# Optimization experiments

Hardware: AMD Instinct MI355X
Metric: run time of the kernel (lower is better)

The kernel has to match this reference:

```python
import jax, jax.numpy as jnp
import numpy as np

D_EMB = 1024
N_HEADS = 16
HEAD_SIZE = 64
LN_EPS = 1e-5


def _layernorm(x, g, b):
    mu = jnp.mean(x, axis=-1, keepdims=True)
    var = jnp.var(x, axis=-1, keepdims=True)
    return (x - mu) * jax.lax.rsqrt(var + LN_EPS) * g + b


def setup_inputs() -> dict:
    key = jax.random.key(0)
    ks = jax.random.split(key, 16)
    B, N, D, H, HS = 8, 1024, D_EMB, N_HEADS, HEAD_SIZE
    s_in = 1.0 / np.sqrt(D)
    s_h = 1.0 / np.sqrt(H * HS)
    s_ff = 1.0 / np.sqrt(4 * D)
    return {
        "x": jax.random.normal(ks[0], (B, N, D), jnp.float32),
        # per-head q/k/v projections, stacked over heads: [H, D, HS]
        "Wq": jax.random.normal(ks[1], (H, D, HS), jnp.float32) * s_in,
        "bq": jnp.zeros((H, HS), jnp.float32),
        "Wk": jax.random.normal(ks[2], (H, D, HS), jnp.float32) * s_in,
        "bk": jnp.zeros((H, HS), jnp.float32),
        "Wv": jax.random.normal(ks[3], (H, D, HS), jnp.float32) * s_in,
        "bv": jnp.zeros((H, HS), jnp.float32),
        "Wproj": jax.random.normal(ks[4], (H * HS, D), jnp.float32) * s_h,
        "bproj": jnp.zeros((D,), jnp.float32),
        "W1": jax.random.normal(ks[5], (D, 4 * D), jnp.float32) * s_in,
        "b1": jnp.zeros((4 * D,), jnp.float32),
        "W2": jax.random.normal(ks[6], (4 * D, D), jnp.float32) * s_ff,
        "b2": jnp.zeros((D,), jnp.float32),
        "ln1_g": jnp.ones((D,), jnp.float32),
        "ln1_b": jnp.zeros((D,), jnp.float32),
        "ln2_g": jnp.ones((D,), jnp.float32),
        "ln2_b": jnp.zeros((D,), jnp.float32),
    }


def reference(x, Wq, bq, Wk, bk, Wv, bv, Wproj, bproj, W1, b1, W2, b2,
              ln1_g, ln1_b, ln2_g, ln2_b):
    # --- pre-LN multi-head attention (dropout = identity in eval) ---
    h = _layernorm(x, ln1_g, ln1_b)                    # [B, N, D]
    q = jnp.einsum('bnd,hds->bhns', h, Wq) + bq[None, :, None, :]
    k = jnp.einsum('bnd,hds->bhns', h, Wk) + bk[None, :, None, :]
    v = jnp.einsum('bnd,hds->bhns', h, Wv) + bv[None, :, None, :]
    scale = 1.0 / jnp.sqrt(jnp.float32(HEAD_SIZE))
    wei = jnp.einsum('bhns,bhms->bhnm', q, k) * scale  # [B, H, N, N]
    wei = jax.nn.softmax(wei, axis=-1)
    attn = jnp.einsum('bhnm,bhms->bhns', wei, v)       # [B, H, N, HS]
    B, H, N, HS = attn.shape
    attn = attn.transpose(0, 2, 1, 3).reshape(B, N, H * HS)  # concat heads
    x = x + attn @ Wproj + bproj
    # --- pre-LN feed-forward with LeakyReLU ---
    h2 = _layernorm(x, ln2_g, ln2_b)
    ff = jax.nn.leaky_relu(h2 @ W1 + b1, negative_slope=0.01) @ W2 + b2
    return x + ff
```

## Files before the change

kernel.cpp:

```cpp
#include <hip/hip_runtime.h>
#include <cstdint>
#include <cstddef>

typedef unsigned short u16;
typedef __attribute__((ext_vector_type(4))) float f32x4;
typedef __attribute__((ext_vector_type(8))) short s16x8;

#define D_EMB 1024
#define NSEQ 1024
#define NB 8
#define NH 16
#define HS 64
#define DFF 4096
#define MTOT (NB*NSEQ)

__device__ __forceinline__ u16 f2bf(float f){
  unsigned u = __float_as_uint(f);
  u += 0x7FFFu + ((u >> 16) & 1u);
  return (u16)(u >> 16);
}
__device__ __forceinline__ u16 bft(float f){ return (u16)(__float_as_uint(f) >> 16); }

__device__ __forceinline__ void gload_lds16(const void* g, void* l){
  __builtin_amdgcn_global_load_lds((const __attribute__((address_space(1))) void*)g,
                                   (__attribute__((address_space(3))) void*)l, 16, 0, 0);
}

__global__ void transpose_cvt(const float* __restrict__ in, u16* __restrict__ out,
                              int R, int C, size_t inStride, size_t outStride){
  __shared__ float t[32][33];
  const float* ip = in + (size_t)blockIdx.z * inStride;
  u16* op = out + (size_t)blockIdx.z * outStride;
  int c0 = blockIdx.x * 32, r0 = blockIdx.y * 32;
  int tx = threadIdx.x, ty = threadIdx.y;
#pragma unroll
  for (int j = 0; j < 32; j += 8)
    t[ty + j][tx] = ip[(size_t)(r0 + ty + j) * C + (c0 + tx)];
  __syncthreads();
#pragma unroll
  for (int j = 0; j < 32; j += 8)
    op[(size_t)(c0 + ty + j) * R + (r0 + tx)] = f2bf(t[tx][ty + j]);
}

__global__ __launch_bounds__(256) void ln_kernel(const float* __restrict__ x,
    const float* __restrict__ g, const float* __restrict__ bb, u16* __restrict__ out){
  int row = blockIdx.x;
  const float* xr = x + (size_t)row * D_EMB;
  int c = threadIdx.x * 4;
  f32x4 v = *(const f32x4*)(xr + c);
  float s1 = v[0] + v[1] + v[2] + v[3];
  float s2 = v[0]*v[0] + v[1]*v[1] + v[2]*v[2] + v[3]*v[3];
#pragma unroll
  for (int m = 32; m > 0; m >>= 1){ s1 += __shfl_xor(s1, m); s2 += __shfl_xor(s2, m); }
  __shared__ float ps1[4], ps2[4];
  int w = threadIdx.x >> 6;
  if ((threadIdx.x & 63) == 0){ ps1[w] = s1; ps2[w] = s2; }
  __syncthreads();
  s1 = ps1[0] + ps1[1] + ps1[2] + ps1[3];
  s2 = ps2[0] + ps2[1] + ps2[2] + ps2[3];
  float mu = s1 * (1.f / D_EMB);
  float var = s2 * (1.f / D_EMB) - mu * mu;
  float rs = rsqrtf(var + 1e-5f);
  ushort4 o;
  o.x = f2bf((v[0]-mu)*rs*g[c+0] + bb[c+0]);
  o.y = f2bf((v[1]-mu)*rs*g[c+1] + bb[c+1]);
  o.z = f2bf((v[2]-mu)*rs*g[c+2] + bb[c+2]);
  o.w = f2bf((v[3]-mu)*rs*g[c+3] + bb[c+3]);
  *(ushort4*)(out + (size_t)row * D_EMB + c) = o;
}

template<int MODE, int BMT, int BNT, int NTHR>
__global__ __launch_bounds__(NTHR) void gemm2ph(
    const u16* __restrict__ A, const u16* __restrict__ Bt,
    int M, int N, int K,
    const float* __restrict__ bias0, const float* __restrict__ bias1,
    const float* __restrict__ bias2, const float* __restrict__ resid,
    void* __restrict__ o0, void* __restrict__ o1, void* __restrict__ o2)
{
  constexpr int NWAVE = NTHR/64;
  constexpr int WCN = BNT/64, WRN = NWAVE/WCN;
  constexpr int WROWS = BMT/WRN;
  constexpr int RF = WROWS/16;
  static_assert(RF*16*WRN == BMT, "wave tiling must cover BMT");
  constexpr int RPP = NTHR/4;
  constexpr int ALD = (BMT*32)/(NTHR*8);
  constexpr int BLD = (BNT*32)/(NTHR*8);
  __shared__ alignas(16) u16 Al[2][BMT*32];
  __shared__ alignas(16) u16 Bl[2][BNT*32];

  const int tid = threadIdx.x;
  const int wid = tid>>6, lane = tid&63, lr = lane&15, lg = lane>>4;
  const int wr = wid/WCN, wc = wid%WCN;

  const int gx = gridDim.x;
  const int gy = gridDim.y;
  const int nwg = gx * gy;
  const int bid = blockIdx.x + blockIdx.y*gx;
  const int wg = (bid&7)*(nwg>>3) + (bid>>3);
  const int m0 = (wg / gy) * BMT;
  const int n0 = (wg % gy) * BNT;

  const int srow = tid>>2;
  const int scs = (((tid&3) - ((srow>>1)&3)) & 3) * 8;

  auto stage = [&](int buf, int kt){
    const u16* asrc = A + (size_t)(m0 + srow)*K + kt*32 + scs;
#pragma unroll
    for (int r = 0; r < ALD; ++r)
      gload_lds16(asrc + (size_t)(r*RPP)*K, &Al[buf][r*(NTHR*8) + tid*8]);
    const u16* bsrc = Bt + (size_t)(n0 + srow)*K + kt*32 + scs;
#pragma unroll
    for (int r = 0; r < BLD; ++r)
      gload_lds16(bsrc + (size_t)(r*RPP)*K, &Bl[buf][r*(NTHR*8) + tid*8]);
  };

  f32x4 acc[RF][4];
#pragma unroll
  for (int i = 0; i < RF; i++)
#pragma unroll
    for (int j = 0; j < 4; j++) acc[i][j] = {0.f,0.f,0.f,0.f};

  const int nk = K/32;
  stage(0, 0);
  for (int kt = 0; kt < nk; ++kt){
    __syncthreads();
    if (kt + 1 < nk) stage((kt+1)&1, kt+1);
    const int buf = kt & 1;
    s16x8 af[RF], bf[4];
#pragma unroll
    for (int i = 0; i < RF; i++){
      const int ar = wr*WROWS + i*16 + lr;
      af[i] = *(const s16x8*)&Al[buf][ar*32 + (((lg + (ar>>1)) & 3)<<3)];
    }
#pragma unroll
    for (int j = 0; j < 4; j++){
      const int br = wc*64 + j*16 + lr;
      bf[j] = *(const s16x8*)&Bl[buf][br*32 + (((lg + (br>>1)) & 3)<<3)];
    }
#pragma unroll
    for (int i = 0; i < RF; i++)
#pragma unroll
      for (int j = 0; j < 4; j++)
        acc[i][j] = __builtin_amdgcn_mfma_f32_16x16x32_bf16(af[i], bf[j], acc[i][j], 0, 0, 0);
  }

#pragma unroll
  for (int fm = 0; fm < RF; fm++){
    const int gmb = m0 + wr*WROWS + fm*16 + lg*4;
#pragma unroll
    for (int fn = 0; fn < 4; fn++){
      const int gn = n0 + wc*64 + fn*16 + lr;
#pragma unroll
      for (int i = 0; i < 4; i++){
        const int gm = gmb + i;
        float v = acc[fm][fn][i];
        if (MODE == 0){
          const int cls = gn >> 10, nn = gn & 1023;
          if (cls == 0)      ((u16*)o0)[(size_t)gm * D_EMB + nn] = f2bf((v + bias0[nn]) * 0.18033688f);
          else if (cls == 1) ((u16*)o1)[(size_t)gm * D_EMB + nn] = f2bf(v + bias1[nn]);
          else {
            const int hh = nn >> 6, ss = nn & 63, bb = gm >> 10, tt = gm & 1023;
            ((u16*)o2)[(((size_t)(bb * NH + hh)) * HS + ss) * NSEQ + tt] = f2bf(v + bias2[nn]);
          }
        } else if (MODE == 1){
          ((float*)o0)[(size_t)gm * N + gn] = resid[(size_t)gm * N + gn] + v + bias0[gn];
        } else {
          float y = v + bias0[gn];
          y = y > 0.f ? y : 0.01f * y;
          ((u16*)o0)[(size_t)gm * N + gn] = f2bf(y);
        }
      }
    }
  }
}

__global__ __launch_bounds__(256) void attn_kernel(
    const u16* __restrict__ Qb, const u16* __restrict__ Kb, const u16* __restrict__ VT,
    u16* __restrict__ attnC)
{
  const int bid = blockIdx.x;
  const int bh = bid & 127, qt = bid >> 7;
  const int b = bh >> 4, h = bh & 15;
  const int tid = threadIdx.x, w = tid >> 6, lane = tid & 63;
  const int lr = lane & 15, lg = lane >> 4;
  const int q0 = qt * 128 + w * 32;

  __shared__ alignas(16) u16 Kl[2][64*64];
  __shared__ alignas(16) u16 Vl[2][64*64];
  __shared__ alignas(16) u16 Pl[4][32][72];

  const int srow = tid >> 3, scg = tid & 7;
  const u16* kbase = Kb + (size_t)(b * NSEQ) * D_EMB + h * HS;
  const u16* vbase = VT + ((size_t)(b * NH + h)) * HS * NSEQ;

  auto stage = [&](int buf, int kt){
    const int tk = kt * 64;
#pragma unroll
    for (int p = 0; p < 2; ++p){
      const int row = srow + p * 32;
      const int sc = scg ^ (row & 7);
      gload_lds16(kbase + (size_t)(tk + row) * D_EMB + sc * 8, &Kl[buf][(p * 256 + tid) * 8]);
      gload_lds16(vbase + (size_t)row * NSEQ + tk + sc * 8,    &Vl[buf][(p * 256 + tid) * 8]);
    }
  };

  s16x8 aq[2][2];
#pragma unroll
  for (int rb = 0; rb < 2; rb++)
#pragma unroll
    for (int kh = 0; kh < 2; kh++)
      aq[rb][kh] = *(const s16x8*)(Qb + (size_t)(b * NSEQ + q0 + rb * 16 + lr) * D_EMB
                                   + h * HS + kh * 32 + lg * 8);

  float m_i[2][4], l_i[2][4];
  f32x4 zero = {0.f, 0.f, 0.f, 0.f};
  f32x4 ao[2][4];
#pragma unroll
  for (int rb = 0; rb < 2; rb++)
#pragma unroll
    for (int i = 0; i < 4; i++){ m_i[rb][i] = -1e30f; l_i[rb][i] = 0.f; ao[rb][i] = zero; }

  const int rsw = lr & 7;

  stage(0, 0);
  for (int kt = 0; kt < NSEQ / 64; ++kt){
    __syncthreads();
    if (kt + 1 < NSEQ / 64) stage((kt + 1) & 1, kt + 1);
    const int cur = kt & 1;

    f32x4 sv[2][4];
#pragma unroll
    for (int rb = 0; rb < 2; rb++)
#pragma unroll
      for (int fn = 0; fn < 4; fn++) sv[rb][fn] = zero;
#pragma unroll
    for (int fn = 0; fn < 4; fn++){
      const int krow = fn * 16 + lr;
#pragma unroll
      for (int kh = 0; kh < 2; kh++){
        const int chunk = (kh * 4 + lg) ^ rsw;
        s16x8 kf = *(const s16x8*)&Kl[cur][krow * 64 + chunk * 8];
        sv[0][fn] = __builtin_amdgcn_mfma_f32_16x16x32_bf16(aq[0][kh], kf, sv[0][fn], 0, 0, 0);
        sv[1][fn] = __builtin_amdgcn_mfma_f32_16x16x32_bf16(aq[1][kh], kf, sv[1][fn], 0, 0, 0);
      }
    }

#pragma unroll
    for (int rb = 0; rb < 2; rb++){
      float p[4][4];
#pragma unroll
      for (int i = 0; i < 4; i++){
        float s0 = sv[rb][0][i], s1 = sv[rb][1][i];
        float s2 = sv[rb][2][i], s3 = sv[rb][3][i];
        float lmax = fmaxf(fmaxf(s0, s1), fmaxf(s2, s3));
        if (__any(lmax > m_i[rb][i] + 8.0f)){
          float rmax = lmax;
#pragma unroll
          for (int mm = 8; mm > 0; mm >>= 1) rmax = fmaxf(rmax, __shfl_xor(rmax, mm));
          float mnew = fmaxf(m_i[rb][i], rmax);
          float fac = exp2f(m_i[rb][i] - mnew);
          l_i[rb][i] *= fac;
#pragma unroll
          for (int fn = 0; fn < 4; fn++) ao[rb][fn][i] *= fac;
          m_i[rb][i] = mnew;
        }
        const float m = m_i[rb][i];
        float p0 = exp2f(s0 - m), p1 = exp2f(s1 - m);
        float p2 = exp2f(s2 - m), p3 = exp2f(s3 - m);
        p[0][i] = p0; p[1][i] = p1; p[2][i] = p2; p[3][i] = p3;
        l_i[rb][i] += (p0 + p1) + (p2 + p3);
      }
#pragma unroll
      for (int fn = 0; fn < 4; fn++)
#pragma unroll
        for (int i = 0; i < 4; i++)
          Pl[w][rb * 16 + lg * 4 + i][fn * 16 + lr] = bft(p[fn][i]);
    }

    s16x8 vf[4][2];
#pragma unroll
    for (int fn = 0; fn < 4; fn++){
      const int vrow = fn * 16 + lr;
#pragma unroll
      for (int kh = 0; kh < 2; kh++){
        const int chunk = (kh * 4 + lg) ^ rsw;
        vf[fn][kh] = *(const s16x8*)&Vl[cur][vrow * 64 + chunk * 8];
      }
    }
#pragma unroll
    for (int rb = 0; rb < 2; rb++){
      s16x8 pa0 = *(const s16x8*)&Pl[w][rb * 16 + lr][lg * 8];
      s16x8 pa1 = *(const s16x8*)&Pl[w][rb * 16 + lr][32 + lg * 8];
#pragma unroll
      for (int fn = 0; fn < 4; fn++){
        ao[rb][fn] = __builtin_amdgcn_mfma_f32_16x16x32_bf16(pa0, vf[fn][0], ao[rb][fn], 0, 0, 0);
        ao[rb][fn] = __builtin_amdgcn_mfma_f32_16x16x32_bf16(pa1, vf[fn][1], ao[rb][fn], 0, 0, 0);
      }
    }
  }

#pragma unroll
  for (int rb = 0; rb < 2; rb++)
#pragma unroll
    for (int i = 0; i < 4; i++)
#pragma unroll
      for (int mm = 8; mm > 0; mm >>= 1) l_i[rb][i] += __shfl_xor(l_i[rb][i], mm);

#pragma unroll
  for (int rb = 0; rb < 2; rb++)
#pragma unroll
    for (int fn = 0; fn < 4; fn++)
#pragma unroll
      for (int i = 0; i < 4; i++){
        float v = ao[rb][fn][i] / l_i[rb][i];
        attnC[(size_t)(b * NSEQ + q0 + rb * 16 + lg * 4 + i) * D_EMB + h * HS + fn * 16 + lr] = f2bf(v);
      }
}

extern "C" void kernel_launch(void* const* d_in, const int* in_sizes, int n_in,
                              void* d_out, int out_size, void* d_ws, size_t ws_size,
                              hipStream_t stream)
{
  const float* x    = (const float*)d_in[0];
  const float* Wq   = (const float*)d_in[1];
  const float* bq   = (const float*)d_in[2];
  const float* Wk   = (const float*)d_in[3];
  const float* bk   = (const float*)d_in[4];
  const float* Wv   = (const float*)d_in[5];
  const float* bv   = (const float*)d_in[6];
  const float* Wp   = (const float*)d_in[7];
  const float* bp   = (const float*)d_in[8];
  const float* W1   = (const float*)d_in[9];
  const float* b1   = (const float*)d_in[10];
  const float* W2   = (const float*)d_in[11];
  const float* b2   = (const float*)d_in[12];
  const float* ln1g = (const float*)d_in[13];
  const float* ln1b = (const float*)d_in[14];
  const float* ln2g = (const float*)d_in[15];
  const float* ln2b = (const float*)d_in[16];
  float* out = (float*)d_out;

  char* ws = (char*)d_ws;
  size_t off = 0;
  auto mk = [&](size_t bytes)->void*{ void* p = ws + off; off += (bytes + 255) & ~(size_t)255; return p; };
  u16*  h1    = (u16*) mk((size_t)MTOT * D_EMB * 2);
  u16*  Qb    = (u16*) mk((size_t)MTOT * D_EMB * 2);
  u16*  Kb    = (u16*) mk((size_t)MTOT * D_EMB * 2);
  u16*  VTb   = (u16*) mk((size_t)MTOT * D_EMB * 2);
  u16*  attnC = (u16*) mk((size_t)MTOT * D_EMB * 2);
  float* x1   = (float*)mk((size_t)MTOT * D_EMB * 4);
  u16*  h2    = (u16*) mk((size_t)MTOT * D_EMB * 2);
  u16*  ffb   = (u16*) mk((size_t)MTOT * DFF * 2);
  u16*  WqkvT = (u16*) mk((size_t)3 * D_EMB * D_EMB * 2);
  u16*  WpT   = (u16*) mk((size_t)D_EMB * D_EMB * 2);
  u16*  W1T   = (u16*) mk((size_t)D_EMB * DFF * 2);
  u16*  W2T   = (u16*) mk((size_t)D_EMB * DFF * 2);

  dim3 tb(32, 8, 1);
  transpose_cvt<<<dim3(HS/32, D_EMB/32, NH), tb, 0, stream>>>(Wq, WqkvT,                         D_EMB, HS, (size_t)D_EMB*HS, (size_t)HS*D_EMB);
  transpose_cvt<<<dim3(HS/32, D_EMB/32, NH), tb, 0, stream>>>(Wk, WqkvT + (size_t)D_EMB*D_EMB,   D_EMB, HS, (size_t)D_EMB*HS, (size_t)HS*D_EMB);
  transpose_cvt<<<dim3(HS/32, D_EMB/32, NH), tb, 0, stream>>>(Wv, WqkvT + (size_t)2*D_EMB*D_EMB, D_EMB, HS, (size_t)D_EMB*HS, (size_t)HS*D_EMB);
  transpose_cvt<<<dim3(D_EMB/32, D_EMB/32, 1), tb, 0, stream>>>(Wp, WpT,  D_EMB, D_EMB, 0, 0);
  transpose_cvt<<<dim3(DFF/32,  D_EMB/32, 1), tb, 0, stream>>>(W1, W1T,  D_EMB, DFF,   0, 0);
  transpose_cvt<<<dim3(D_EMB/32, DFF/32,  1), tb, 0, stream>>>(W2, W2T,  DFF,   D_EMB, 0, 0);

  ln_kernel<<<MTOT, 256, 0, stream>>>(x, ln1g, ln1b, h1);

  gemm2ph<0,128,256,512><<<dim3(MTOT/128, 3*D_EMB/256), 512, 0, stream>>>(
      h1, WqkvT, MTOT, 3*D_EMB, D_EMB, bq, bk, bv, nullptr, Qb, Kb, VTb);

  attn_kernel<<<NB*NH*(NSEQ/128), 256, 0, stream>>>(Qb, Kb, VTb, attnC);

  gemm2ph<1,64,128,256><<<dim3(MTOT/64, D_EMB/128), 256, 0, stream>>>(
      attnC, WpT, MTOT, D_EMB, D_EMB, bp, nullptr, nullptr, x, x1, nullptr, nullptr);

  ln_kernel<<<MTOT, 256, 0, stream>>>(x1, ln2g, ln2b, h2);

  gemm2ph<2,128,256,512><<<dim3(MTOT/128, DFF/256), 512, 0, stream>>>(
      h2, W1T, MTOT, DFF, D_EMB, b1, nullptr, nullptr, nullptr, ffb, nullptr, nullptr);

  gemm2ph<1,64,128,256><<<dim3(MTOT/64, D_EMB/128), 256, 0, stream>>>(
      ffb, W2T, MTOT, D_EMB, DFF, b2, nullptr, nullptr, x1, out, nullptr, nullptr);
}
```

Before: 434.4 us.

## Add 256x256-tile GEMM with 4-stage LDS pipeline for QKV and FFN1

Adds a new GEMM kernel using 256x256 output tiles, 128 KB of dynamic LDS, a 4-deep global-to-LDS prefetch ring with vmcnt-based waits, and an XCD-aware block remapping. It replaces the 128x256 kernel for the QKV projection and the first FFN matmul. The larger tile raises arithmetic intensity and the deeper pipeline hides load latency, at the cost of one workgroup per CU and fewer blocks (e.g. 384 for QKV), which can hurt wave quantization. It falls back to the old kernel if the LDS attribute cannot be set.

Measured after the change: 458.7 us. +5.6%, slower.

```diff
diff --git a/kernel.cpp b/kernel.cpp
--- a/kernel.cpp
+++ b/kernel.cpp
@@ -25,6 +25,8 @@
   __builtin_amdgcn_global_load_lds((const __attribute__((address_space(1))) void*)g,
                                    (__attribute__((address_space(3))) void*)l, 16, 0, 0);
 }
+
+#define WAITV(n) asm volatile("s_waitcnt vmcnt(" #n ")" ::: "memory")
 
 __global__ void transpose_cvt(const float* __restrict__ in, u16* __restrict__ out,
                               int R, int C, size_t inStride, size_t outStride){
@@ -67,6 +69,133 @@
   o.z = f2bf((v[2]-mu)*rs*g[c+2] + bb[c+2]);
   o.w = f2bf((v[3]-mu)*rs*g[c+3] + bb[c+3]);
   *(ushort4*)(out + (size_t)row * D_EMB + c) = o;
+}
+
+template<int MODE>
+__global__ __launch_bounds__(512) void gemm256(
+    const u16* __restrict__ A, const u16* __restrict__ Bt,
+    int M, int N, int K,
+    const float* __restrict__ bias0, const float* __restrict__ bias1,
+    const float* __restrict__ bias2, const float* __restrict__ resid,
+    void* __restrict__ o0, void* __restrict__ o1, void* __restrict__ o2)
+{
+  constexpr int BMT = 256, BNT = 256;
+  constexpr int WCN = 4, WROWS = 128;
+  constexpr int RF = 8, RH = 4;
+  constexpr int ABUF = BMT*32, BBUF = BNT*32;
+  extern __shared__ u16 lds[];
+  u16* const Ab = lds;
+  u16* const Bb = lds + 4*ABUF;
+
+  const int tid = threadIdx.x;
+  const int wid = tid>>6, lane = tid&63, lr = lane&15, lg = lane>>4;
+  const int wr = wid/WCN, wc = wid%WCN;
+
+  const int gx = gridDim.x;
+  const int gy = gridDim.y;
+  const int nwg = gx * gy;
+  const int bid = blockIdx.x + blockIdx.y*gx;
+  const int wg = (bid&7)*(nwg>>3) + (bid>>3);
+  const int m0 = (wg / gy) * BMT;
+  const int n0 = (wg % gy) * BNT;
+
+  const int nkt = K/32;
+  const int srow = tid>>2;
+  const int scs = (((tid&3) - ((srow>>1)&3)) & 3) * 8;
+
+  auto stageA = [&](int kt3){
+    const u16* src = A + (size_t)(m0 + srow)*K + kt3*32 + scs;
+    u16* dst = Ab + (kt3&3)*ABUF + tid*8;
+    gload_lds16(src, dst);
+    gload_lds16(src + (size_t)128*K, dst + 4096);
+  };
+  auto stageB = [&](int kt3){
+    const u16* src = Bt + (size_t)(n0 + srow)*K + kt3*32 + scs;
+    u16* dst = Bb + (kt3&3)*BBUF + tid*8;
+    gload_lds16(src, dst);
+    gload_lds16(src + (size_t)128*K, dst + 4096);
+  };
+  auto rdA = [&](int kt, int fm) -> s16x8 {
+    const int row = wr*WROWS + fm*16 + lr;
+    return *(const s16x8*)&Ab[(kt&3)*ABUF + row*32 + (((lg + (row>>1)) & 3)<<3)];
+  };
+  auto rdB = [&](int kt, int fn) -> s16x8 {
+    const int row = wc*64 + fn*16 + lr;
+    return *(const s16x8*)&Bb[(kt&3)*BBUF + row*32 + (((lg + (row>>1)) & 3)<<3)];
+  };
+
+  f32x4 acc[RF][4];
+#pragma unroll
+  for (int i = 0; i < RF; i++)
+#pragma unroll
+    for (int j = 0; j < 4; j++) acc[i][j] = {0.f,0.f,0.f,0.f};
+
+  auto tile = [&](int kt, bool doStage, int wsel){
+    s16x8 af[RH], bf[4];
+#pragma unroll
+    for (int f = 0; f < 4;  ++f) bf[f] = rdB(kt, f);
+#pragma unroll
+    for (int j = 0; j < RH; ++j) af[j] = rdA(kt, j);
+    if (doStage){ stageA(kt+3); stageB(kt+3); }
+    __builtin_amdgcn_s_setprio(1);
+#pragma unroll
+    for (int j = 0; j < RH; ++j)
+#pragma unroll
+      for (int f = 0; f < 4; ++f)
+        acc[j][f] = __builtin_amdgcn_mfma_f32_16x16x32_bf16(af[j], bf[f], acc[j][f], 0, 0, 0);
+    __builtin_amdgcn_s_setprio(0);
+#pragma unroll
+    for (int j = 0; j < RH; ++j) af[j] = rdA(kt, RH + j);
+    __builtin_amdgcn_s_setprio(1);
+#pragma unroll
+    for (int j = 0; j < RH; ++j)
+#pragma unroll
+      for (int f = 0; f < 4; ++f)
+        acc[RH+j][f] = __builtin_amdgcn_mfma_f32_16x16x32_bf16(af[j], bf[f], acc[RH+j][f], 0, 0, 0);
+    __builtin_amdgcn_s_setprio(0);
+    if (wsel == 2)      WAITV(8);
+    else if (wsel == 1) WAITV(4);
+    else if (wsel == 0) WAITV(0);
+    if (wsel >= 0) __builtin_amdgcn_s_barrier();
+  };
+
+  stageA(0); stageB(0);
+  stageA(1); stageB(1);
+  stageA(2); stageB(2);
+  WAITV(8);
+  __builtin_amdgcn_s_barrier();
+
+  for (int kt = 0; kt < nkt - 3; ++kt) tile(kt, true, 2);
+  tile(nkt-3, false, 1);
+  tile(nkt-2, false, 0);
+  tile(nkt-1, false, -1);
+
+#pragma unroll
+  for (int fm = 0; fm < RF; fm++){
+    const int gmb = m0 + wr*WROWS + fm*16 + lg*4;
+#pragma unroll
+    for (int fn = 0; fn < 4; fn++){
+      const int gn = n0 + wc*64 + fn*16 + lr;
+#pragma unroll
+      for (int i = 0; i < 4; i++){
+        const int gm = gmb + i;
+        float v = acc[fm][fn][i];
+        if (MODE == 0){
+          const int cls = gn >> 10, nn = gn & 1023;
+          if (cls == 0)      ((u16*)o0)[(size_t)gm * D_EMB + nn] = f2bf((v + bias0[nn]) * 0.18033688f);
+          else if (cls == 1) ((u16*)o1)[(size_t)gm * D_EMB + nn] = f2bf(v + bias1[nn]);
+          else {
+            const int hh = nn >> 6, ss = nn & 63, bb = gm >> 10, tt = gm & 1023;
+            ((u16*)o2)[(((size_t)(bb * NH + hh)) * HS + ss) * NSEQ + tt] = f2bf(v + bias2[nn]);
+          }
+        } else {
+          float y = v + bias0[gn];
+          y = y > 0.f ? y : 0.01f * y;
+          ((u16*)o0)[(size_t)gm * N + gn] = f2bf(y);
+        }
+      }
+    }
+  }
 }
 
 template<int MODE, int BMT, int BNT, int NTHR>
@@ -366,8 +495,19 @@
 
   ln_kernel<<<MTOT, 256, 0, stream>>>(x, ln1g, ln1b, h1);
 
-  gemm2ph<0,128,256,512><<<dim3(MTOT/128, 3*D_EMB/256), 512, 0, stream>>>(
-      h1, WqkvT, MTOT, 3*D_EMB, D_EMB, bq, bk, bv, nullptr, Qb, Kb, VTb);
+  bool big = true;
+  big &= hipFuncSetAttribute(reinterpret_cast<const void*>(&gemm256<0>),
+                             hipFuncAttributeMaxDynamicSharedMemorySize, 131072) == hipSuccess;
+  big &= hipFuncSetAttribute(reinterpret_cast<const void*>(&gemm256<2>),
+                             hipFuncAttributeMaxDynamicSharedMemorySize, 131072) == hipSuccess;
+
+  if (big){
+    gemm256<0><<<dim3(MTOT/256, 3*D_EMB/256), 512, 131072, stream>>>(
+        h1, WqkvT, MTOT, 3*D_EMB, D_EMB, bq, bk, bv, nullptr, Qb, Kb, VTb);
+  } else {
+    gemm2ph<0,128,256,512><<<dim3(MTOT/128, 3*D_EMB/256), 512, 0, stream>>>(
+        h1, WqkvT, MTOT, 3*D_EMB, D_EMB, bq, bk, bv, nullptr, Qb, Kb, VTb);
+  }
 
   attn_kernel<<<NB*NH*(NSEQ/128), 256, 0, stream>>>(Qb, Kb, VTb, attnC);
 
@@ -376,8 +516,13 @@
 
   ln_kernel<<<MTOT, 256, 0, stream>>>(x1, ln2g, ln2b, h2);
 
-  gemm2ph<2,128,256,512><<<dim3(MTOT/128, DFF/256), 512, 0, stream>>>(
-      h2, W1T, MTOT, DFF, D_EMB, b1, nullptr, nullptr, nullptr, ffb, nullptr, nullptr);
+  if (big){
+    gemm256<2><<<dim3(MTOT/256, DFF/256), 512, 131072, stream>>>(
+        h2, W1T, MTOT, DFF, D_EMB, b1, nullptr, nullptr, nullptr, ffb, nullptr, nullptr);
+  } else {
+    gemm2ph<2,128,256,512><<<dim3(MTOT/128, DFF/256), 512, 0, stream>>>(
+        h2, W1T, MTOT, DFF, D_EMB, b1, nullptr, nullptr, nullptr, ffb, nullptr, nullptr);
+  }
 
   gemm2ph<1,64,128,256><<<dim3(MTOT/64, D_EMB/128), 256, 0, stream>>>(
       ffb, W2T, MTOT, D_EMB, DFF, b2, nullptr, nullptr, x1, out, nullptr, nullptr);
```
